# Performance work log

Hardware: AMD Instinct MI355X
Metric: run time of the kernel (lower is better)

Reference implementation:

```python
import jax, jax.numpy as jnp
import numpy as np

HEAD_DIM = 64
KERNEL_EPS = 1e-3  # lucidrains generalized_kernel kernel_epsilon


def setup_inputs() -> dict:
    key = jax.random.key(0)
    k1, k2, k3, k4 = jax.random.split(key, 4)
    B, H, N, D, R = 4, 8, 4096, HEAD_DIM, 256
    return {
        "Q": jax.random.normal(k1, (B, H, N, D), dtype=jnp.float32),
        "K": jax.random.normal(k2, (B, H, N, D), dtype=jnp.float32),
        "V": jax.random.normal(k3, (B, H, N, D), dtype=jnp.float32),
        "mask": jnp.ones((B, N), dtype=jnp.float32),
        "proj": jax.random.normal(k4, (R, D), dtype=jnp.float32),
    }


def reference(Q, K, V, mask, proj):
    # PerformerAttention.forward: scale Q,K by d^{-1/4}, zero out masked keys/values
    scale = 1.0 / jnp.sqrt(jnp.sqrt(jnp.float32(HEAD_DIM)))
    m = mask[:, None, :, None]               # [B,1,N,1]
    q = Q * scale
    k = K * scale * m
    v = V * m

    # generalized random-feature map phi(x) = relu(x @ proj^T) + eps  -> [B,H,N,R]
    phi_q = jax.nn.relu(jnp.einsum('bhnd,rd->bhnr', q, proj)) + KERNEL_EPS
    phi_k = jax.nn.relu(jnp.einsum('bhnd,rd->bhnr', k, proj)) + KERNEL_EPS

    # non-causal linear attention: out = phi_q (phi_k^T v) / (phi_q (phi_k^T 1))
    k_sum = phi_k.sum(axis=2)                                  # [B,H,R]
    d_inv = 1.0 / jnp.einsum('bhnr,bhr->bhn', phi_q, k_sum)    # [B,H,N]
    context = jnp.einsum('bhnr,bhnd->bhrd', phi_k, v)          # [B,H,R,D]
    out = jnp.einsum('bhnr,bhrd->bhnd', phi_q, context) * d_inv[..., None]
    return out
```

## Files before the change

### kernel.cpp

```cpp
#include <hip/hip_runtime.h>
#include <hip/hip_bf16.h>

#define BB 4
#define HH 8
#define NN 4096
#define DD 64
#define RR 256

constexpr float SCALE = 0.35355339059327373f;
constexpr float KEPS  = 0.001f;

typedef __attribute__((ext_vector_type(8)))  short short8;
typedef __attribute__((ext_vector_type(16))) float f32x16;

#define MFMA(a, b, c) __builtin_amdgcn_mfma_f32_32x32x16_bf16(a, b, c, 0, 0, 0)

union S8U { short8 s; uint4 u; };

__device__ inline unsigned bfpk(float a, float b) {
    __hip_bfloat162 h = __float22bfloat162_rn(make_float2(a, b));
    return *reinterpret_cast<unsigned*>(&h);
}
__device__ inline f32x16 fz16() {
    f32x16 z;
#pragma unroll
    for (int e = 0; e < 16; ++e) z[e] = 0.f;
    return z;
}

__global__ __launch_bounds__(256)
void prep_proj(const float* __restrict__ proj, unsigned short* __restrict__ projb)
{
    const int i = (blockIdx.x * 256 + threadIdx.x) * 4;
    const float4 v = *(const float4*)(proj + i);
    uint2 o; o.x = bfpk(v.x * SCALE, v.y * SCALE); o.y = bfpk(v.z * SCALE, v.w * SCALE);
    *(uint2*)(projb + i) = o;
}

__global__ __launch_bounds__(256, 3)
void pk_ctx_kernel(const float* __restrict__ Kmat, const float* __restrict__ Vmat,
                   const float* __restrict__ mask, const unsigned short* __restrict__ projb,
                   float* __restrict__ g_ctxT, float* __restrict__ g_ksum)
{
    __shared__ unsigned short kt[2][32 * 72];
    __shared__ unsigned short vt[2][32 * 68];

    const int tid = threadIdx.x;
    const int w = tid >> 6, lane = tid & 63;
    const int l31 = lane & 31, hf = lane >> 5;
    const int b = blockIdx.z, h = blockIdx.y;
    const int bh = b * HH + h;
    const int nc = blockIdx.x >> 1, rhalf = blockIdx.x & 1;
    const int n0 = nc * 256;
    const int rg = rhalf * 128 + w * 32 + l31;

    const int sn = tid >> 3, sc = (tid & 7) * 8;
    const long rowbase = ((long)bh * NN + n0 + sn) * DD + sc;
    const int  mbase   = b * NN + n0 + sn;

    short8 pfrag[4];
#pragma unroll
    for (int ks = 0; ks < 4; ++ks)
        pfrag[ks] = *(const short8*)(projb + rg * DD + ks * 16 + hf * 8);

    f32x16 acc[2];
    acc[0] = fz16(); acc[1] = fz16();
    float ksum = 0.f;

    auto stage = [&](int buf, int sub) {
        const long off = rowbase + (long)sub * 32 * DD;
        const float m = mask[mbase + sub * 32];
        const float4 ka = *(const float4*)(Kmat + off);
        const float4 kc = *(const float4*)(Kmat + off + 4);
        S8U t; t.u = make_uint4(bfpk(ka.x * m, ka.y * m), bfpk(ka.z * m, ka.w * m),
                                bfpk(kc.x * m, kc.y * m), bfpk(kc.z * m, kc.w * m));
        *(short8*)&kt[buf][sn * 72 + sc] = t.s;
        const float4 va = *(const float4*)(Vmat + off);
        const float4 vc = *(const float4*)(Vmat + off + 4);
        *(uint2*)&vt[buf][sn * 68 + sc]     = make_uint2(bfpk(va.x * m, va.y * m), bfpk(va.z * m, va.w * m));
        *(uint2*)&vt[buf][sn * 68 + sc + 4] = make_uint2(bfpk(vc.x * m, vc.y * m), bfpk(vc.z * m, vc.w * m));
    };

    stage(0, 0);
    __syncthreads();

    for (int sub = 0; sub < 8; ++sub) {
        const int buf = sub & 1;
        if (sub < 7) stage(buf ^ 1, sub + 1);

        short8 afr[4];
#pragma unroll
        for (int ks = 0; ks < 4; ++ks)
            afr[ks] = *(const short8*)&kt[buf][l31 * 72 + ks * 16 + hf * 8];
        f32x16 p = fz16();
#pragma unroll
        for (int ks = 0; ks < 4; ++ks) p = MFMA(afr[ks], pfrag[ks], p);

        unsigned own[8];
#pragma unroll
        for (int g = 0; g < 4; ++g) {
            const float p0 = fmaxf(p[4*g+0], 0.f) + KEPS;
            const float p1 = fmaxf(p[4*g+1], 0.f) + KEPS;
            const float p2 = fmaxf(p[4*g+2], 0.f) + KEPS;
            const float p3 = fmaxf(p[4*g+3], 0.f) + KEPS;
            ksum += (p0 + p1) + (p2 + p3);
            own[2*g]   = bfpk(p0, p1);
            own[2*g+1] = bfpk(p2, p3);
        }
        unsigned par[8];
#pragma unroll
        for (int q = 0; q < 8; ++q) par[q] = (unsigned)__shfl_xor((int)own[q], 32, 64);

#pragma unroll
        for (int kk = 0; kk < 2; ++kk) {
            S8U bf;
            if (hf == 0) bf.u = make_uint4(own[4*kk],   own[4*kk+1], par[4*kk],   par[4*kk+1]);
            else         bf.u = make_uint4(par[4*kk+2], par[4*kk+3], own[4*kk+2], own[4*kk+3]);
#pragma unroll
            for (int mt = 0; mt < 2; ++mt) {
                short8 av;
#pragma unroll
                for (int j = 0; j < 8; ++j)
                    av[j] = (short)vt[buf][(kk * 16 + hf * 8 + j) * 68 + mt * 32 + l31];
                acc[mt] = MFMA(av, bf.s, acc[mt]);
            }
        }
        __syncthreads();
    }

#pragma unroll
    for (int mt = 0; mt < 2; ++mt)
#pragma unroll
        for (int i = 0; i < 16; ++i) {
            const int drow = mt * 32 + (i & 3) + 8 * (i >> 2) + 4 * hf;
            atomicAdd(g_ctxT + ((long)bh * DD + drow) * RR + rhalf * 128 + w * 32 + l31,
                      acc[mt][i]);
        }
    const float kst = ksum + __shfl_xor(ksum, 32, 64);
    if (hf == 0) atomicAdd(g_ksum + bh * RR + rhalf * 128 + w * 32 + l31, kst);
}

__global__ __launch_bounds__(256, 3)
void out_kernel(const float* __restrict__ Qmat, const unsigned short* __restrict__ projb,
                const float* __restrict__ g_ctxT, const float* __restrict__ g_ksum,
                float* __restrict__ out)
{
    __shared__ float ks_lds[RR];

    const int tid = threadIdx.x;
    const int w = tid >> 6, lane = tid & 63;
    const int l31 = lane & 31, hf = lane >> 5;
    const int bh = blockIdx.z * HH + blockIdx.y;
    const int n0 = blockIdx.x * 128;
    const int nl = w * 32 + l31;

    ks_lds[tid] = g_ksum[bh * RR + tid];

    const long qrow = ((long)bh * NN + n0 + nl) * DD;
    short8 qfr[4];
#pragma unroll
    for (int ks = 0; ks < 4; ++ks) {
        const float4 a = *(const float4*)(Qmat + qrow + ks * 16 + hf * 8);
        const float4 c = *(const float4*)(Qmat + qrow + ks * 16 + hf * 8 + 4);
        S8U t; t.u = make_uint4(bfpk(a.x, a.y), bfpk(a.z, a.w), bfpk(c.x, c.y), bfpk(c.z, c.w));
        qfr[ks] = t.s;
    }
    __syncthreads();

    f32x16 cacc[2];
    cacc[0] = fz16(); cacc[1] = fz16();
    float s_acc = 0.f;

    for (int rt = 0; rt < 8; ++rt) {
        f32x16 p = fz16();
#pragma unroll
        for (int ks = 0; ks < 4; ++ks) {
            const short8 af = *(const short8*)(projb + (rt * 32 + l31) * DD + ks * 16 + hf * 8);
            p = MFMA(af, qfr[ks], p);
        }
        unsigned own[8];
#pragma unroll
        for (int g = 0; g < 4; ++g) {
            const float4 kv = *(const float4*)&ks_lds[rt * 32 + 8 * g + 4 * hf];
            const float p0 = fmaxf(p[4*g+0], 0.f) + KEPS; s_acc = fmaf(p0, kv.x, s_acc);
            const float p1 = fmaxf(p[4*g+1], 0.f) + KEPS; s_acc = fmaf(p1, kv.y, s_acc);
            const float p2 = fmaxf(p[4*g+2], 0.f) + KEPS; s_acc = fmaf(p2, kv.z, s_acc);
            const float p3 = fmaxf(p[4*g+3], 0.f) + KEPS; s_acc = fmaf(p3, kv.w, s_acc);
            own[2*g]   = bfpk(p0, p1);
            own[2*g+1] = bfpk(p2, p3);
        }
        unsigned par[8];
#pragma unroll
        for (int q = 0; q < 8; ++q) par[q] = (unsigned)__shfl_xor((int)own[q], 32, 64);

#pragma unroll
        for (int kk = 0; kk < 2; ++kk) {
            S8U a;
            if (hf == 0) a.u = make_uint4(own[4*kk],   own[4*kk+1], par[4*kk],   par[4*kk+1]);
            else         a.u = make_uint4(par[4*kk+2], par[4*kk+3], own[4*kk+2], own[4*kk+3]);
#pragma unroll
            for (int dt = 0; dt < 2; ++dt) {
                const float* cp = g_ctxT + ((long)bh * DD + dt * 32 + l31) * RR
                                         + rt * 32 + kk * 16 + hf * 8;
                const float4 x = *(const float4*)cp;
                const float4 y = *(const float4*)(cp + 4);
                S8U bfr; bfr.u = make_uint4(bfpk(x.x, x.y), bfpk(x.z, x.w),
                                            bfpk(y.x, y.y), bfpk(y.z, y.w));
                cacc[dt] = MFMA(a.s, bfr.s, cacc[dt]);
            }
        }
    }

    const float st = s_acc + __shfl_xor(s_acc, 32, 64);
    const float sinv = 1.0f / st;
#pragma unroll
    for (int i = 0; i < 16; ++i) {
        const int row = (i & 3) + 8 * (i >> 2) + 4 * hf;
        const float sv = __shfl(sinv, row, 64);
#pragma unroll
        for (int dt = 0; dt < 2; ++dt)
            out[((long)bh * NN + n0 + w * 32 + row) * DD + dt * 32 + l31] = cacc[dt][i] * sv;
    }
}

extern "C" void kernel_launch(void* const* d_in, const int* in_sizes, int n_in,
                              void* d_out, int out_size, void* d_ws, size_t ws_size,
                              hipStream_t stream)
{
    const float* Q    = (const float*)d_in[0];
    const float* K    = (const float*)d_in[1];
    const float* V    = (const float*)d_in[2];
    const float* mask = (const float*)d_in[3];
    const float* proj = (const float*)d_in[4];
    float* out = (float*)d_out;

    float* g_ctxT = (float*)d_ws;
    float* g_ksum = g_ctxT + (size_t)BB * HH * DD * RR;
    unsigned short* projb = (unsigned short*)(g_ksum + (size_t)BB * HH * RR);

    const size_t zbytes = ((size_t)BB * HH * DD * RR + (size_t)BB * HH * RR) * sizeof(float);
    hipMemsetAsync(d_ws, 0, zbytes, stream);

    prep_proj<<<dim3(RR * DD / 1024), 256, 0, stream>>>(proj, projb);

    dim3 g1((NN / 256) * 2, HH, BB);
    pk_ctx_kernel<<<g1, 256, 0, stream>>>(K, V, mask, projb, g_ctxT, g_ksum);

    dim3 g2(NN / 128, HH, BB);
    out_kernel<<<g2, 256, 0, stream>>>(Q, projb, g_ctxT, g_ksum, out);
}
```

Before: 209.8 us.

## Transpose V staging in LDS and prefetch context tiles in output kernel

```diff
diff --git a/kernel.cpp b/kernel.cpp
--- a/kernel.cpp
+++ b/kernel.cpp
@@ -42,8 +42,8 @@
                    const float* __restrict__ mask, const unsigned short* __restrict__ projb,
                    float* __restrict__ g_ctxT, float* __restrict__ g_ksum)
 {
-    __shared__ unsigned short kt[2][32 * 72];
-    __shared__ unsigned short vt[2][32 * 68];
+    __shared__ __align__(16) unsigned short kt[2][32 * 68];
+    __shared__ __align__(16) unsigned short vt[2][64 * 36];
 
     const int tid = threadIdx.x;
     const int w = tid >> 6, lane = tid & 63;
@@ -55,8 +55,11 @@
     const int rg = rhalf * 128 + w * 32 + l31;
 
     const int sn = tid >> 3, sc = (tid & 7) * 8;
-    const long rowbase = ((long)bh * NN + n0 + sn) * DD + sc;
-    const int  mbase   = b * NN + n0 + sn;
+    const long krow = ((long)bh * NN + n0 + sn) * DD + sc;
+    const int  mrow = b * NN + n0 + sn;
+    const int dcol = tid & 63, ngrp = tid >> 6;
+    const long vcol = ((long)bh * NN + n0 + ngrp * 8) * DD + dcol;
+    const int  mgrp = b * NN + n0 + ngrp * 8;
 
     short8 pfrag[4];
 #pragma unroll
@@ -68,17 +71,24 @@
     float ksum = 0.f;
 
     auto stage = [&](int buf, int sub) {
-        const long off = rowbase + (long)sub * 32 * DD;
-        const float m = mask[mbase + sub * 32];
-        const float4 ka = *(const float4*)(Kmat + off);
-        const float4 kc = *(const float4*)(Kmat + off + 4);
-        S8U t; t.u = make_uint4(bfpk(ka.x * m, ka.y * m), bfpk(ka.z * m, ka.w * m),
-                                bfpk(kc.x * m, kc.y * m), bfpk(kc.z * m, kc.w * m));
-        *(short8*)&kt[buf][sn * 72 + sc] = t.s;
-        const float4 va = *(const float4*)(Vmat + off);
-        const float4 vc = *(const float4*)(Vmat + off + 4);
-        *(uint2*)&vt[buf][sn * 68 + sc]     = make_uint2(bfpk(va.x * m, va.y * m), bfpk(va.z * m, va.w * m));
-        *(uint2*)&vt[buf][sn * 68 + sc + 4] = make_uint2(bfpk(vc.x * m, vc.y * m), bfpk(vc.z * m, vc.w * m));
+        const long koff = krow + (long)sub * 32 * DD;
+        const float m = mask[mrow + sub * 32];
+        const float4 ka = *(const float4*)(Kmat + koff);
+        const float4 kc = *(const float4*)(Kmat + koff + 4);
+        *(uint2*)&kt[buf][sn * 68 + sc] =
+            make_uint2(bfpk(ka.x * m, ka.y * m), bfpk(ka.z * m, ka.w * m));
+        *(uint2*)&kt[buf][sn * 68 + sc + 4] =
+            make_uint2(bfpk(kc.x * m, kc.y * m), bfpk(kc.z * m, kc.w * m));
+        const long voff = vcol + (long)sub * 32 * DD;
+        float vv[8];
+#pragma unroll
+        for (int j = 0; j < 8; ++j) vv[j] = Vmat[voff + (long)j * DD];
+        const float4 ma = *(const float4*)(mask + mgrp + sub * 32);
+        const float4 mb = *(const float4*)(mask + mgrp + sub * 32 + 4);
+        *(uint2*)&vt[buf][dcol * 36 + ngrp * 8] =
+            make_uint2(bfpk(vv[0] * ma.x, vv[1] * ma.y), bfpk(vv[2] * ma.z, vv[3] * ma.w));
+        *(uint2*)&vt[buf][dcol * 36 + ngrp * 8 + 4] =
+            make_uint2(bfpk(vv[4] * mb.x, vv[5] * mb.y), bfpk(vv[6] * mb.z, vv[7] * mb.w));
     };
 
     stage(0, 0);
@@ -88,13 +98,14 @@
         const int buf = sub & 1;
         if (sub < 7) stage(buf ^ 1, sub + 1);
 
-        short8 afr[4];
-#pragma unroll
-        for (int ks = 0; ks < 4; ++ks)
-            afr[ks] = *(const short8*)&kt[buf][l31 * 72 + ks * 16 + hf * 8];
         f32x16 p = fz16();
 #pragma unroll
-        for (int ks = 0; ks < 4; ++ks) p = MFMA(afr[ks], pfrag[ks], p);
+        for (int ks = 0; ks < 4; ++ks) {
+            const uint2 lo = *(const uint2*)&kt[buf][l31 * 68 + ks * 16 + hf * 8];
+            const uint2 hi = *(const uint2*)&kt[buf][l31 * 68 + ks * 16 + hf * 8 + 4];
+            S8U a; a.u = make_uint4(lo.x, lo.y, hi.x, hi.y);
+            p = MFMA(a.s, pfrag[ks], p);
+        }
 
         unsigned own[8];
 #pragma unroll
@@ -118,11 +129,11 @@
             else         bf.u = make_uint4(par[4*kk+2], par[4*kk+3], own[4*kk+2], own[4*kk+3]);
 #pragma unroll
             for (int mt = 0; mt < 2; ++mt) {
-                short8 av;
-#pragma unroll
-                for (int j = 0; j < 8; ++j)
-                    av[j] = (short)vt[buf][(kk * 16 + hf * 8 + j) * 68 + mt * 32 + l31];
-                acc[mt] = MFMA(av, bf.s, acc[mt]);
+                const int vbase = (mt * 32 + l31) * 36 + kk * 16 + hf * 8;
+                const uint2 lo = *(const uint2*)&vt[buf][vbase];
+                const uint2 hi = *(const uint2*)&vt[buf][vbase + 4];
+                S8U av; av.u = make_uint4(lo.x, lo.y, hi.x, hi.y);
+                acc[mt] = MFMA(av.s, bf.s, acc[mt]);
             }
         }
         __syncthreads();
@@ -165,6 +176,33 @@
         S8U t; t.u = make_uint4(bfpk(a.x, a.y), bfpk(a.z, a.w), bfpk(c.x, c.y), bfpk(c.z, c.w));
         qfr[ks] = t.s;
     }
+
+    const float* ctxbase = g_ctxT + (long)bh * DD * RR + (long)l31 * RR;
+
+    float4 nc[8];
+    auto load_ctx = [&](int rt) {
+#pragma unroll
+        for (int kk = 0; kk < 2; ++kk)
+#pragma unroll
+            for (int dt = 0; dt < 2; ++dt) {
+                const float* cp = ctxbase + (long)dt * 32 * RR + rt * 32 + kk * 16 + hf * 8;
+                nc[(kk * 2 + dt) * 2]     = *(const float4*)cp;
+                nc[(kk * 2 + dt) * 2 + 1] = *(const float4*)(cp + 4);
+            }
+    };
+    short8 cf[4];
+    auto pack_ctx = [&]() {
+#pragma unroll
+        for (int q = 0; q < 4; ++q) {
+            const float4 x = nc[q * 2], y = nc[q * 2 + 1];
+            S8U t; t.u = make_uint4(bfpk(x.x, x.y), bfpk(x.z, x.w),
+                                    bfpk(y.x, y.y), bfpk(y.z, y.w));
+            cf[q] = t.s;
+        }
+    };
+
+    load_ctx(0);
+    pack_ctx();
     __syncthreads();
 
     f32x16 cacc[2];
@@ -172,6 +210,8 @@
     float s_acc = 0.f;
 
     for (int rt = 0; rt < 8; ++rt) {
+        if (rt < 7) load_ctx(rt + 1);
+
         f32x16 p = fz16();
 #pragma unroll
         for (int ks = 0; ks < 4; ++ks) {
@@ -198,17 +238,10 @@
             S8U a;
             if (hf == 0) a.u = make_uint4(own[4*kk],   own[4*kk+1], par[4*kk],   par[4*kk+1]);
             else         a.u = make_uint4(par[4*kk+2], par[4*kk+3], own[4*kk+2], own[4*kk+3]);
-#pragma unroll
-            for (int dt = 0; dt < 2; ++dt) {
-                const float* cp = g_ctxT + ((long)bh * DD + dt * 32 + l31) * RR
-                                         + rt * 32 + kk * 16 + hf * 8;
-                const float4 x = *(const float4*)cp;
-                const float4 y = *(const float4*)(cp + 4);
-                S8U bfr; bfr.u = make_uint4(bfpk(x.x, x.y), bfpk(x.z, x.w),
-                                            bfpk(y.x, y.y), bfpk(y.z, y.w));
-                cacc[dt] = MFMA(a.s, bfr.s, cacc[dt]);
-            }
-        }
+            cacc[0] = MFMA(a.s, cf[kk * 2 + 0], cacc[0]);
+            cacc[1] = MFMA(a.s, cf[kk * 2 + 1], cacc[1]);
+        }
+        if (rt < 7) pack_ctx();
     }
 
     const float st = s_acc + __shfl_xor(s_acc, 32, 64);
```

Result: slower. 255.6 us (+21.8%).
